# Kernel optimization log

Hardware: AMD Instinct MI355X
Metric: run time of the kernel (lower is better)

Reference implementation:

```python
import jax, jax.numpy as jnp
import numpy as np

SEQ_LEN = 4096
NUM_EIGH = 40
D_IN = 64
D_OUT = 64
K_U = 3
BSZ = 2


def _spectral_filters(L, K):
    # Hankel matrix Z_ij = 2/((i+j)^3 - (i+j)), i,j in [1, L]
    e = np.arange(1, L + 1, dtype=np.float64)
    s = e[:, None] + e[None, :]
    Z = 2.0 / (s ** 3 - s)
    sigma, phi = np.linalg.eigh(Z)
    phi_k = phi[:, -K:] * sigma[-K:] ** 0.25  # (L, K)
    return jnp.asarray(phi_k, dtype=jnp.float32)


def setup_inputs() -> dict:
    key = jax.random.key(0)
    kx, km, kp, kn = jax.random.split(key, 4)
    x = jax.random.normal(kx, (BSZ, SEQ_LEN, D_IN), dtype=jnp.float32)
    phi = _spectral_filters(SEQ_LEN, NUM_EIGH)  # (L, K)
    M = jax.random.normal(km, (D_OUT, D_IN, K_U), dtype=jnp.float32) / D_IN
    M_phi_plus = jax.random.normal(kp, (NUM_EIGH, D_IN, D_OUT), dtype=jnp.float32) / 10.0
    M_phi_minus = jax.random.normal(kn, (NUM_EIGH, D_IN, D_OUT), dtype=jnp.float32) / 10.0
    return {"x": x, "phi": phi, "M": M, "M_phi_plus": M_phi_plus, "M_phi_minus": M_phi_minus}


def _stu_forward(x, phi, M, M_phi_plus, M_phi_minus):
    bsz, L, d_in = x.shape
    n = int(2 ** np.ceil(np.log2(2 * L - 1)))  # FFT length (8192)
    t = jnp.arange(L)
    sgn = jnp.where(t % 2 == 1, -1.0, 1.0).astype(x.dtype)  # (L,)

    # FFT of [u, u*sgn] once over d_in (K-expansion deferred to freq domain; FFT is linear)
    U = jnp.stack([x, x * sgn[None, :, None]], axis=-1)        # (b, L, d, 2)
    U_f = jnp.fft.rfft(U, n=n, axis=1)                         # (b, nf, d, 2)
    v_f = jnp.fft.rfft(phi.astype(jnp.float32), n=n, axis=0)   # (nf, K)

    prod = v_f[None, :, :, None, None] * U_f[:, :, None, :, :]  # (b, nf, K, d, 2)
    U_conv = jnp.fft.irfft(prod, n=n, axis=1)[:, :L]            # (b, L, K, d, 2)
    U_plus = U_conv[..., 0]
    U_minus = U_conv[..., 1] * sgn[None, :, None, None]

    # spectral tensordot: contract (K, d_in) -> d_out
    spec = (jnp.einsum('blkd,kdo->blo', U_plus, M_phi_plus)
            + jnp.einsum('blkd,kdo->blo', U_minus, M_phi_minus))

    ar = jnp.zeros((bsz, L, M.shape[0]), dtype=x.dtype)
    for i in range(M.shape[2]):  # k_u is small and fixed
        y_i = jnp.einsum('bli,oi->blo', x, M[:, :, i])
        if i > 0:
            y_i = jnp.pad(y_i[:, : L - i], ((0, 0), (i, 0), (0, 0)))
        ar = ar + y_i
    return spec + ar


def reference(x, phi, M, M_phi_plus, M_phi_minus):
    return _stu_forward(x, phi, M, M_phi_plus, M_phi_minus)
```

## Files before the change

### kernel.cpp

```cpp
#include <hip/hip_runtime.h>

typedef short bf16x8 __attribute__((ext_vector_type(8)));
typedef float f32x4 __attribute__((ext_vector_type(4)));
typedef float f32x16 __attribute__((ext_vector_type(16)));
typedef unsigned short u16;

__device__ __forceinline__ u16 f2bf(float f) {
    unsigned u = __builtin_bit_cast(unsigned, f);
    return (u16)((u + 0x7fffu + ((u >> 16) & 1u)) >> 16);
}

__global__ void k_prep(const float* __restrict__ x, u16* __restrict__ xpad,
                       const float* __restrict__ Mp, const float* __restrict__ Mm,
                       float* __restrict__ ApT, float* __restrict__ AmT) {
    __shared__ float tp[64 * 65], tm[64 * 65];
    if (blockIdx.x < 1024) {
        int gid = blockIdx.x * 256 + threadIdx.x;
        int b   = gid >> 17;
        int rem = gid & 131071;
        int r   = rem >> 4;
        int c4  = rem & 15;
        u16 o0 = 0, o1 = 0, o2 = 0, o3 = 0;
        if (r >= 4096) {
            const f32x4 v = *(const f32x4*)(x + ((b << 12) + (r - 4096)) * 64 + c4 * 4);
            o0 = f2bf(v.x); o1 = f2bf(v.y); o2 = f2bf(v.z); o3 = f2bf(v.w);
        }
        u16* p = xpad + ((b << 13) + r) * 64 + c4 * 4;
        p[0] = o0; p[1] = o1; p[2] = o2; p[3] = o3;
    } else {
        const int k = blockIdx.x - 1024, tid = threadIdx.x;
        for (int f = tid; f < 4096; f += 256) {
            int d = f >> 6, o = f & 63;
            float p = Mp[k * 4096 + f], m = Mm[k * 4096 + f];
            tp[o * 65 + d] = p + m;
            tm[o * 65 + d] = p - m;
        }
        __syncthreads();
        for (int f = tid; f < 4096; f += 256) {
            int o = f >> 6, d = f & 63;
            ApT[k * 4096 + f] = tp[o * 65 + d];
            AmT[k * 4096 + f] = tm[o * 65 + d];
        }
    }
}

__global__ __launch_bounds__(256)
void k_build_w(const float* __restrict__ phi, const float* __restrict__ ApT,
               const float* __restrict__ AmT, const float* __restrict__ Mar,
               u16* __restrict__ wg) {
    const int sb = blockIdx.x;
    const int qb = blockIdx.y;
    const int s0 = sb * 64;
    const int q  = qb * 256 + threadIdx.x;
    const int o  = q >> 6, d = q & 63;

    float ap[40], am[40];
    #pragma unroll
    for (int k = 0; k < 40; ++k) { ap[k] = ApT[k * 4096 + q]; am[k] = AmT[k * 4096 + q]; }

    for (int j = 0; j < 64; j += 2) {
        const float* ph = phi + (s0 + j) * 40;
        float a0 = 0.f, a1 = 0.f, b0 = 0.f, b1 = 0.f;
        #pragma unroll
        for (int k = 0; k < 40; k += 2) { a0 += ph[k] * ap[k]; a1 += ph[k + 1] * ap[k + 1]; }
        #pragma unroll
        for (int k = 0; k < 40; k += 2) { b0 += ph[40 + k] * am[k]; b1 += ph[41 + k] * am[k + 1]; }
        float ev = a0 + a1, ov = b0 + b1;
        int s = s0 + j;
        if (s < 3)     ev += Mar[o * 192 + d * 3 + s];
        if (s + 1 < 3) ov += Mar[o * 192 + d * 3 + s + 1];
        wg[(size_t)s * 4096 + q]       = f2bf(ev);
        wg[(size_t)(s + 1) * 4096 + q] = f2bf(ov);
    }
}

__global__ __launch_bounds__(256, 2)
void k_spectral(const u16* __restrict__ xpad, const u16* __restrict__ wg,
                float* __restrict__ out, int* __restrict__ counter) {
    __shared__ __align__(16) u16 xs[2 * 192 * 64];
    __shared__ __align__(16) u16 wsm[2 * 64 * 64];
    __shared__ int sh;

    const int tid  = threadIdx.x;
    const int lane = tid & 63, w = tid >> 6;
    const int m31  = lane & 31, g2 = lane >> 5;
    const int batch = w >> 1, tb_loc = (w & 1) << 6;
    const int fo0 = (tid * 2) >> 3, fc0 = (tid * 2) & 7;
    const int fo1 = (tid * 2 + 1) >> 3, fc1 = (tid * 2 + 1) & 7;

    for (;;) {
        __syncthreads();
        if (tid == 0) sh = atomicAdd(counter, 1);
        __syncthreads();
        const int U = sh;
        if (U >= 1056) break;

        int I = (int)((sqrtf(4.f * (float)U + 1.f) - 1.f) * 0.5f);
        while ((I + 1) * (I + 2) <= U) ++I;
        while (I * (I + 1) > U) --I;
        const int J = U - I * (I + 1);
        const int t0 = I << 7, s0 = J << 6;
        const int base = 4096 + t0 - s0 - 63;

        #pragma unroll
        for (int b = 0; b < 2; ++b) {
            #pragma unroll
            for (int ii = 0; ii < 6; ++ii) {
                int f = tid + ii * 256;
                int r = f >> 3, c = f & 7;
                int g = base + r;
                if (g > 8191) g = 8191;
                bf16x8 v = *(const bf16x8*)(xpad + ((b << 13) + g) * 64 + c * 8);
                *(bf16x8*)(xs + ((b * 192 + r) * 8 + (c ^ (r & 7))) * 8) = v;
            }
        }
        bf16x8 pre0 = *(const bf16x8*)(wg + (size_t)s0 * 4096 + (tid * 2) * 8);
        bf16x8 pre1 = *(const bf16x8*)(wg + (size_t)s0 * 4096 + (tid * 2 + 1) * 8);

        f32x16 acc[2][2];
        #pragma unroll
        for (int mt = 0; mt < 2; ++mt)
            #pragma unroll
            for (int nt = 0; nt < 2; ++nt)
                acc[mt][nt] = (f32x16)(0.f);

        const u16* xbase = xs + batch * (192 * 64);

        #pragma unroll 2
        for (int ds = 0; ds < 64; ++ds) {
            const int bufo = (ds & 1) * 4096;
            *(bf16x8*)(wsm + bufo + (fo0 * 8 + (fc0 ^ (fo0 & 7))) * 8) = pre0;
            *(bf16x8*)(wsm + bufo + (fo1 * 8 + (fc1 ^ (fo1 & 7))) * 8) = pre1;
            __syncthreads();
            if (ds < 63) {
                const u16* wp = wg + (size_t)(s0 + ds + 1) * 4096;
                pre0 = *(const bf16x8*)(wp + (tid * 2) * 8);
                pre1 = *(const bf16x8*)(wp + (tid * 2 + 1) * 8);
            }
            const int rb = tb_loc + m31 + 63 - ds;
            bf16x8 af[2][4], bfr[2][4];
            #pragma unroll
            for (int mt = 0; mt < 2; ++mt) {
                int r = rb + mt * 32;
                #pragma unroll
                for (int ks = 0; ks < 4; ++ks) {
                    int c = (ks * 2 + g2) ^ (r & 7);
                    af[mt][ks] = *(const bf16x8*)(xbase + (r * 8 + c) * 8);
                }
            }
            #pragma unroll
            for (int nt = 0; nt < 2; ++nt) {
                int o = nt * 32 + m31;
                #pragma unroll
                for (int ks = 0; ks < 4; ++ks) {
                    int c = (ks * 2 + g2) ^ (o & 7);
                    bfr[nt][ks] = *(const bf16x8*)(wsm + bufo + (o * 8 + c) * 8);
                }
            }
            #pragma unroll
            for (int ks = 0; ks < 4; ++ks)
                #pragma unroll
                for (int mt = 0; mt < 2; ++mt)
                    #pragma unroll
                    for (int nt = 0; nt < 2; ++nt)
                        acc[mt][nt] = __builtin_amdgcn_mfma_f32_32x32x16_bf16(
                            af[mt][ks], bfr[nt][ks], acc[mt][nt], 0, 0, 0);
        }

        #pragma unroll
        for (int mt = 0; mt < 2; ++mt) {
            #pragma unroll
            for (int nt = 0; nt < 2; ++nt) {
                int o = nt * 32 + m31;
                #pragma unroll
                for (int i = 0; i < 16; ++i) {
                    int row = (i & 3) + 8 * (i >> 2) + 4 * g2;
                    int t = t0 + tb_loc + mt * 32 + row;
                    atomicAdd(out + ((batch << 12) + t) * 64 + o, acc[mt][nt][i]);
                }
            }
        }
    }
}

extern "C" void kernel_launch(void* const* d_in, const int* in_sizes, int n_in,
                              void* d_out, int out_size, void* d_ws, size_t ws_size,
                              hipStream_t stream) {
    const float* x   = (const float*)d_in[0];
    const float* phi = (const float*)d_in[1];
    const float* M   = (const float*)d_in[2];
    const float* Mp  = (const float*)d_in[3];
    const float* Mm  = (const float*)d_in[4];
    float* out = (float*)d_out;

    int* counter = (int*)d_ws;
    u16* xpad = (u16*)((char*)d_ws + 4096);
    u16* wg   = (u16*)((char*)d_ws + 4096 + 2097152);
    float* ApT = (float*)((char*)d_ws + 4096 + 2097152 + 33554432);
    float* AmT = ApT + 40 * 4096;

    hipMemsetAsync(d_ws, 0, 4, stream);
    hipMemsetAsync(d_out, 0, 2 * 4096 * 64 * sizeof(float), stream);
    k_prep<<<1064, 256, 0, stream>>>(x, xpad, Mp, Mm, ApT, AmT);
    k_build_w<<<dim3(64, 16), 256, 0, stream>>>(phi, ApT, AmT, M, wg);
    k_spectral<<<512, 256, 0, stream>>>(xpad, wg, out, counter);
}
```

Measured before the change: 267.9 us.

## Split K across waves with 16x16x32 MFMA tiles and fold memsets into prep

The spectral kernel now splits the 64-wide input-channel reduction between the two waves of each batch. Each wave computes a full 64x128 output tile with 16x16x32 bf16 MFMAs, which cuts LDS fragment loads per MFMA. The cost is twice as many atomicAdds to the output, since both K halves accumulate into the same elements, though lanes now write runs of 4 contiguous floats. The two hipMemsetAsync calls for the output and the work counter are replaced by extra blocks in the prep kernel, removing separate launches.

```diff
diff --git a/kernel.cpp b/kernel.cpp
--- a/kernel.cpp
+++ b/kernel.cpp
@@ -2,7 +2,6 @@
 
 typedef short bf16x8 __attribute__((ext_vector_type(8)));
 typedef float f32x4 __attribute__((ext_vector_type(4)));
-typedef float f32x16 __attribute__((ext_vector_type(16)));
 typedef unsigned short u16;
 
 __device__ __forceinline__ u16 f2bf(float f) {
@@ -12,7 +11,8 @@
 
 __global__ void k_prep(const float* __restrict__ x, u16* __restrict__ xpad,
                        const float* __restrict__ Mp, const float* __restrict__ Mm,
-                       float* __restrict__ ApT, float* __restrict__ AmT) {
+                       float* __restrict__ ApT, float* __restrict__ AmT,
+                       float* __restrict__ out, int* __restrict__ counter) {
     __shared__ float tp[64 * 65], tm[64 * 65];
     if (blockIdx.x < 1024) {
         int gid = blockIdx.x * 256 + threadIdx.x;
@@ -27,7 +27,7 @@
         }
         u16* p = xpad + ((b << 13) + r) * 64 + c4 * 4;
         p[0] = o0; p[1] = o1; p[2] = o2; p[3] = o3;
-    } else {
+    } else if (blockIdx.x < 1064) {
         const int k = blockIdx.x - 1024, tid = threadIdx.x;
         for (int f = tid; f < 4096; f += 256) {
             int d = f >> 6, o = f & 63;
@@ -41,6 +41,13 @@
             ApT[k * 4096 + f] = tp[o * 65 + d];
             AmT[k * 4096 + f] = tm[o * 65 + d];
         }
+    } else {
+        const int bz = blockIdx.x - 1064;
+        if (bz == 0 && threadIdx.x == 0) *counter = 0;
+        float* po = out + bz * 4096;
+        #pragma unroll
+        for (int i = 0; i < 4; ++i)
+            *(f32x4*)(po + (threadIdx.x + i * 256) * 4) = (f32x4){0.f, 0.f, 0.f, 0.f};
     }
 }
 
@@ -83,8 +90,9 @@
 
     const int tid  = threadIdx.x;
     const int lane = tid & 63, w = tid >> 6;
-    const int m31  = lane & 31, g2 = lane >> 5;
-    const int batch = w >> 1, tb_loc = (w & 1) << 6;
+    const int m15  = lane & 15, q4 = lane >> 4;
+    const int batch = w >> 1, kh = w & 1;
+    const int kq = kh * 4 + q4;
     const int fo0 = (tid * 2) >> 3, fc0 = (tid * 2) & 7;
     const int fo1 = (tid * 2 + 1) >> 3, fc1 = (tid * 2 + 1) & 7;
 
@@ -117,12 +125,12 @@
         bf16x8 pre0 = *(const bf16x8*)(wg + (size_t)s0 * 4096 + (tid * 2) * 8);
         bf16x8 pre1 = *(const bf16x8*)(wg + (size_t)s0 * 4096 + (tid * 2 + 1) * 8);
 
-        f32x16 acc[2][2];
-        #pragma unroll
-        for (int mt = 0; mt < 2; ++mt)
-            #pragma unroll
-            for (int nt = 0; nt < 2; ++nt)
-                acc[mt][nt] = (f32x16)(0.f);
+        f32x4 acc[4][8];
+        #pragma unroll
+        for (int mt = 0; mt < 4; ++mt)
+            #pragma unroll
+            for (int nt = 0; nt < 8; ++nt)
+                acc[mt][nt] = (f32x4){0.f, 0.f, 0.f, 0.f};
 
         const u16* xbase = xs + batch * (192 * 64);
 
@@ -137,47 +145,35 @@
                 pre0 = *(const bf16x8*)(wp + (tid * 2) * 8);
                 pre1 = *(const bf16x8*)(wp + (tid * 2 + 1) * 8);
             }
-            const int rb = tb_loc + m31 + 63 - ds;
-            bf16x8 af[2][4], bfr[2][4];
-            #pragma unroll
-            for (int mt = 0; mt < 2; ++mt) {
-                int r = rb + mt * 32;
+            bf16x8 af[4];
+            #pragma unroll
+            for (int mt = 0; mt < 4; ++mt) {
+                int o = mt * 16 + m15;
+                af[mt] = *(const bf16x8*)(wsm + bufo + (o * 8 + (kq ^ (o & 7))) * 8);
+            }
+            const int rb = m15 + 63 - ds;
+            #pragma unroll
+            for (int nt = 0; nt < 8; ++nt) {
+                int r = rb + nt * 16;
+                bf16x8 bfr = *(const bf16x8*)(xbase + (r * 8 + (kq ^ (r & 7))) * 8);
                 #pragma unroll
-                for (int ks = 0; ks < 4; ++ks) {
-                    int c = (ks * 2 + g2) ^ (r & 7);
-                    af[mt][ks] = *(const bf16x8*)(xbase + (r * 8 + c) * 8);
-                }
-            }
-            #pragma unroll
-            for (int nt = 0; nt < 2; ++nt) {
-                int o = nt * 32 + m31;
+                for (int mt = 0; mt < 4; ++mt)
+                    acc[mt][nt] = __builtin_amdgcn_mfma_f32_16x16x32_bf16(
+                        af[mt], bfr, acc[mt][nt], 0, 0, 0);
+            }
+        }
+
+        const int tg = t0 + m15;
+        #pragma unroll
+        for (int mt = 0; mt < 4; ++mt) {
+            int o = mt * 16 + q4 * 4;
+            #pragma unroll
+            for (int nt = 0; nt < 8; ++nt) {
+                int t = tg + nt * 16;
+                float* op = out + ((batch << 12) + t) * 64 + o;
                 #pragma unroll
-                for (int ks = 0; ks < 4; ++ks) {
-                    int c = (ks * 2 + g2) ^ (o & 7);
-                    bfr[nt][ks] = *(const bf16x8*)(wsm + bufo + (o * 8 + c) * 8);
-                }
-            }
-            #pragma unroll
-            for (int ks = 0; ks < 4; ++ks)
-                #pragma unroll
-                for (int mt = 0; mt < 2; ++mt)
-                    #pragma unroll
-                    for (int nt = 0; nt < 2; ++nt)
-                        acc[mt][nt] = __builtin_amdgcn_mfma_f32_32x32x16_bf16(
-                            af[mt][ks], bfr[nt][ks], acc[mt][nt], 0, 0, 0);
-        }
-
-        #pragma unroll
-        for (int mt = 0; mt < 2; ++mt) {
-            #pragma unroll
-            for (int nt = 0; nt < 2; ++nt) {
-                int o = nt * 32 + m31;
-                #pragma unroll
-                for (int i = 0; i < 16; ++i) {
-                    int row = (i & 3) + 8 * (i >> 2) + 4 * g2;
-                    int t = t0 + tb_loc + mt * 32 + row;
-                    atomicAdd(out + ((batch << 12) + t) * 64 + o, acc[mt][nt][i]);
-                }
+                for (int r = 0; r < 4; ++r)
+                    atomicAdd(op + r, acc[mt][nt][r]);
             }
         }
     }
@@ -199,9 +195,7 @@
     float* ApT = (float*)((char*)d_ws + 4096 + 2097152 + 33554432);
     float* AmT = ApT + 40 * 4096;
 
-    hipMemsetAsync(d_ws, 0, 4, stream);
-    hipMemsetAsync(d_out, 0, 2 * 4096 * 64 * sizeof(float), stream);
-    k_prep<<<1064, 256, 0, stream>>>(x, xpad, Mp, Mm, ApT, AmT);
+    k_prep<<<1192, 256, 0, stream>>>(x, xpad, Mp, Mm, ApT, AmT, out, counter);
     k_build_w<<<dim3(64, 16), 256, 0, stream>>>(phi, ApT, AmT, M, wg);
     k_spectral<<<512, 256, 0, stream>>>(xpad, wg, out, counter);
 }
```

Measured after the change: 622.0 us. 2.32x slower.
